# Kernel tuning notes

Hardware: AMD Instinct MI355X
Metric: run time of the kernel (lower is better)

The kernel has to match this reference:

```python
import jax, jax.numpy as jnp
import numpy as np

N, C, H, W = 4, 256, 64, 64  # in_channels == out_channels == C


def conv1x1(x, w, b):
    # x: [N, Cin, H, W], w: [Cout, Cin], b: [Cout]
    return jnp.einsum('nchw,oc->nohw', x, w) + b[None, :, None, None]


def setup_inputs() -> dict:
    key = jax.random.key(0)
    ks = jax.random.split(key, 4)
    scale = 1.0 / np.sqrt(C)
    return {
        'x': jax.random.normal(ks[0], (N, C, H, W), dtype=jnp.float32),
        'theta_w': jax.random.normal(ks[1], (C, C), dtype=jnp.float32) * scale,
        'theta_b': jnp.zeros((C,), dtype=jnp.float32),
        'phi_w': jax.random.normal(ks[2], (C, C), dtype=jnp.float32) * scale,
        'phi_b': jnp.zeros((C,), dtype=jnp.float32),
        'conv1_w': jax.random.normal(ks[3], (C, C), dtype=jnp.float32) * scale,
        'conv1_b': jnp.zeros((C,), dtype=jnp.float32),
    }


def reference(x, theta_w, theta_b, phi_w, phi_b, conv1_w, conv1_b):
    n, c, h, w = x.shape
    hw = h * w
    theta = conv1x1(x, theta_w, theta_b).reshape(n, c, hw)   # queries [N,C,HW]
    phi = conv1x1(x, phi_w, phi_b).reshape(n, c, hw)         # keys    [N,C,HW]
    g = x.reshape(n, c, hw)                                   # values  [N,C,HW]
    # f = einsum('niab,nicd->nabcd') flattened: [N, HW_q, HW_k]
    scores = jnp.einsum('ncp,ncq->npq', theta, phi) / jnp.sqrt(jnp.asarray(c, x.dtype))
    attn = jax.nn.softmax(scores, axis=-1)                    # softmax over keys
    # f = einsum('nabcd,nicd->niab'): weighted sum of values
    f = jnp.einsum('npq,ncq->ncp', attn, g).reshape(n, c, h, w)
    result = conv1x1(f, conv1_w, conv1_b)
    return x + result
```

## Files before the change

### kernel.cpp

```cpp
#include <hip/hip_runtime.h>
#include <hip/hip_bf16.h>

typedef __attribute__((ext_vector_type(8))) short short8;
typedef __attribute__((ext_vector_type(4))) short short4_t;
typedef __attribute__((ext_vector_type(4))) float float4_t;
typedef unsigned short ushort;

#define HW 4096
#define CC 256
#define NBATCH 4
#define SEQ ((size_t)NBATCH * HW)

static __device__ __forceinline__ unsigned short f2b(float f) {
    union { float f; unsigned u; } v; v.f = f;
    unsigned r = v.u + 0x7FFF + ((v.u >> 16) & 1);
    return (unsigned short)(r >> 16);
}
static __device__ __forceinline__ float b2f(unsigned short u) {
    union { unsigned u; float f; } v; v.u = ((unsigned)u) << 16;
    return v.f;
}
static __device__ __forceinline__ unsigned pk2(float a, float b) {
    __hip_bfloat162 h = __float22bfloat162_rn(make_float2(a, b));
    union { __hip_bfloat162 h; unsigned u; } v; v.h = h; return v.u;
}

static __device__ __forceinline__ void barrier_lds() {
    asm volatile("s_waitcnt lgkmcnt(0)" ::: "memory");
    __builtin_amdgcn_s_barrier();
    __builtin_amdgcn_sched_barrier(0);
}

__global__ __launch_bounds__(256) void k_prep(const float* __restrict__ x,
                                              const float* __restrict__ tw,
                                              const float* __restrict__ pw,
                                              const float* __restrict__ cw,
                                              unsigned short* __restrict__ XT,
                                              unsigned short* __restrict__ gb,
                                              unsigned short* __restrict__ Wbt,
                                              unsigned short* __restrict__ Wbp,
                                              unsigned short* __restrict__ Wbc) {
    __shared__ float T[64][65];
    int fb = blockIdx.x + 64 * (blockIdx.y + 4 * blockIdx.z);
    if (fb < 768) {
        int i = fb * 256 + threadIdx.x;
        int sel = i >> 16, off = i & 65535;
        const float* s = sel == 0 ? tw : (sel == 1 ? pw : cw);
        unsigned short* d = sel == 0 ? Wbt : (sel == 1 ? Wbp : Wbc);
        d[off] = f2b(s[off]);
    }
    int n = blockIdx.z, c0 = blockIdx.y * 64, p0 = blockIdx.x * 64;
    int t = threadIdx.x;
    int pl = t & 63, rg = t >> 6;
    const float* xp = x + ((size_t)n * CC + c0) * HW + p0;
    #pragma unroll
    for (int i = 0; i < 16; i++) {
        int cl = rg * 16 + i;
        float v = xp[(size_t)cl * HW + pl];
        T[cl][pl] = v;
        gb[((size_t)n * CC + c0 + cl) * HW + p0 + pl] = f2b(v);
    }
    __syncthreads();
    int cl = t & 63, pg = t >> 6;
    unsigned short* xt = XT + ((size_t)n * HW + p0) * CC + c0;
    #pragma unroll
    for (int i = 0; i < 16; i++) {
        int plw = pg * 16 + i;
        xt[(size_t)plw * CC + cl] = f2b(T[cl][plw]);
    }
}

__global__ __launch_bounds__(256) void k_proj(const unsigned short* __restrict__ XT,
                                              const unsigned short* __restrict__ Wt,
                                              const unsigned short* __restrict__ Wp,
                                              const float* __restrict__ bt,
                                              const float* __restrict__ bp,
                                              unsigned short* __restrict__ outT_t,
                                              unsigned short* __restrict__ outT_p) {
    const unsigned short* W; const float* b; unsigned short* outT;
    if (blockIdx.y == 0) { W = Wt; b = bt; outT = outT_t; }
    else                 { W = Wp; b = bp; outT = outT_p; }
    int w = threadIdx.x >> 6, lane = threadIdx.x & 63;
    int nidx = lane & 15, quad = lane >> 4;
    size_t row0 = (size_t)blockIdx.x * 64 + w * 16;
    float4_t acc[16];
    #pragma unroll
    for (int i = 0; i < 16; i++) acc[i] = (float4_t)(0.f);
    const unsigned short* arow = XT + (row0 + nidx) * CC + quad * 8;
    for (int ks = 0; ks < 8; ks++) {
        short8 a = *(const short8*)(arow + ks * 32);
        #pragma unroll
        for (int cb = 0; cb < 16; cb++) {
            short8 bb = *(const short8*)(W + (size_t)(cb * 16 + nidx) * CC + ks * 32 + quad * 8);
            acc[cb] = __builtin_amdgcn_mfma_f32_16x16x32_bf16(a, bb, acc[cb], 0, 0, 0);
        }
    }
    #pragma unroll
    for (int cb = 0; cb < 16; cb++) {
        int co = cb * 16 + nidx;
        float bias = b[co];
        #pragma unroll
        for (int r = 0; r < 4; r++) {
            size_t prow = row0 + quad * 4 + r;
            outT[prow * CC + co] = f2b(acc[cb][r] + bias);
        }
    }
}

__global__ __launch_bounds__(512)
void k_attn(const unsigned short* __restrict__ thetaT,
            const unsigned short* __restrict__ phiT,
            const unsigned short* __restrict__ gb,
            ushort* __restrict__ Ow, float* __restrict__ lw) {
    __shared__ __align__(16) ushort Kl[2][16384];
    __shared__ __align__(16) ushort Pbuf[2][16][64][8];
    __shared__ float Lbuf[2][128];

    const int tid = threadIdx.x;
    const int w = tid >> 6, lane = tid & 63;
    const int nidx = lane & 15, quad = lane >> 4;
    const int qg = w & 3;
    const int kh = w >> 2;
    const int nb = (blockIdx.x & 7) >> 1;
    const int h  = blockIdx.x & 1;
    const int qtile = blockIdx.x >> 3;
    const int p0 = qtile * 128;
    const size_t seq0 = (size_t)nb * HW;
    const ushort* Kg = phiT + seq0 * CC;
    const ushort* Vg = gb + (size_t)nb * CC * HW;
    const int k00 = h * 2048;

    short8 th[2][8];
    #pragma unroll
    for (int qs = 0; qs < 2; qs++) {
        const ushort* qrow = thetaT + (seq0 + p0 + qg * 32 + qs * 16 + nidx) * CC + quad * 8;
        #pragma unroll
        for (int kb = 0; kb < 8; kb++) th[qs][kb] = *(const short8*)(qrow + kb * 32);
    }

    float4_t o[2][8];
    #pragma unroll
    for (int i = 0; i < 2; i++)
        #pragma unroll
        for (int j = 0; j < 8; j++) o[i][j] = (float4_t)(0.f);
    float lrow[2] = {0.f, 0.f};

    const int c_s = tid >> 4, n_s = tid & 15;
    const int kfbase = (c_s >> 2) * 512 + ((c_s & 3) * 16 + n_s) * 8;
    auto loadKregs = [&](short8 (&kr)[4], int tt) {
        #pragma unroll
        for (int rr = 0; rr < 4; rr++)
            kr[rr] = *(const short8*)(Kg + (size_t)(k00 + tt * 64 + rr * 16 + n_s) * CC + c_s * 8);
    };
    auto stageK = [&](int buf, const short8 (&kr)[4]) {
        #pragma unroll
        for (int rr = 0; rr < 4; rr++) *(short8*)(&Kl[buf][rr * 4096 + kfbase]) = kr[rr];
    };
    auto loadVregs = [&](short8 (&vr)[4], int tt) {
        #pragma unroll
        for (int mg = 0; mg < 2; mg++)
            #pragma unroll
            for (int kst = 0; kst < 2; kst++)
                vr[mg * 2 + kst] = *(const short8*)(Vg + (size_t)(w * 32 + mg * 16 + nidx) * HW
                                                    + k00 + tt * 64 + kst * 32 + quad * 8);
    };

    const float SC = 0.0625f * 1.44269504088896f;
    const int Gp = quad >> 1;
    const int pcell_lo = (nidx ^ (Gp * 4));
    const int pj0 = (quad & 1) * 4;
    const int prcell = ((lane >> 4) << 4) | ((lane & 15) ^ (((lane >> 4) & 1) * 4));

    float4_t s00, s01, s10, s11;
    auto expPhase = [&](int buf) {
        {
            float e0 = exp2f(s00[0] * SC), e1 = exp2f(s00[1] * SC);
            float e2 = exp2f(s00[2] * SC), e3 = exp2f(s00[3] * SC);
            lrow[0] += (e0 + e1) + (e2 + e3);
            uint2 pk; pk.x = pk2(e0, e1); pk.y = pk2(e2, e3);
            *(uint2*)(&Pbuf[buf][(qg * 2 + 0) * 2 + kh][(0 * 2 + Gp) * 16 + pcell_lo][pj0]) = pk;
        }
        {
            float e0 = exp2f(s01[0] * SC), e1 = exp2f(s01[1] * SC);
            float e2 = exp2f(s01[2] * SC), e3 = exp2f(s01[3] * SC);
            lrow[1] += (e0 + e1) + (e2 + e3);
            uint2 pk; pk.x = pk2(e0, e1); pk.y = pk2(e2, e3);
            *(uint2*)(&Pbuf[buf][(qg * 2 + 1) * 2 + kh][(0 * 2 + Gp) * 16 + pcell_lo][pj0]) = pk;
        }
        {
            float e0 = exp2f(s10[0] * SC), e1 = exp2f(s10[1] * SC);
            float e2 = exp2f(s10[2] * SC), e3 = exp2f(s10[3] * SC);
            lrow[0] += (e0 + e1) + (e2 + e3);
            uint2 pk; pk.x = pk2(e0, e1); pk.y = pk2(e2, e3);
            *(uint2*)(&Pbuf[buf][(qg * 2 + 0) * 2 + kh][(1 * 2 + Gp) * 16 + pcell_lo][pj0]) = pk;
        }
        {
            float e0 = exp2f(s11[0] * SC), e1 = exp2f(s11[1] * SC);
            float e2 = exp2f(s11[2] * SC), e3 = exp2f(s11[3] * SC);
            lrow[1] += (e0 + e1) + (e2 + e3);
            uint2 pk; pk.x = pk2(e0, e1); pk.y = pk2(e2, e3);
            *(uint2*)(&Pbuf[buf][(qg * 2 + 1) * 2 + kh][(1 * 2 + Gp) * 16 + pcell_lo][pj0]) = pk;
        }
    };

    short8 kregs[4], vA[4], vB[4];

    auto ITER = [&](int t, const short8 (&vCur)[4], short8 (&vNext)[4]) {
        const int pb = t & 1;
        const int kbuf = (t + 1) & 1;
        s00 = (float4_t)(0.f); s01 = (float4_t)(0.f);
        s10 = (float4_t)(0.f); s11 = (float4_t)(0.f);
        __builtin_amdgcn_s_setprio(1);
        #pragma unroll
        for (int i = 0; i < 8; i++) {
            short8 k0 = *(const short8*)(&Kl[kbuf][((kh * 2 + 0) * 8 + i) * 512 + lane * 8]);
            short8 k1 = *(const short8*)(&Kl[kbuf][((kh * 2 + 1) * 8 + i) * 512 + lane * 8]);
            s00 = __builtin_amdgcn_mfma_f32_16x16x32_bf16(k0, th[0][i], s00, 0, 0, 0);
            s01 = __builtin_amdgcn_mfma_f32_16x16x32_bf16(k0, th[1][i], s01, 0, 0, 0);
            s10 = __builtin_amdgcn_mfma_f32_16x16x32_bf16(k1, th[0][i], s10, 0, 0, 0);
            s11 = __builtin_amdgcn_mfma_f32_16x16x32_bf16(k1, th[1][i], s11, 0, 0, 0);
            short8 pf0 = *(const short8*)(&Pbuf[pb][i * 2 + 0][prcell][0]);
            short8 pf1 = *(const short8*)(&Pbuf[pb][i * 2 + 1][prcell][0]);
            o[0][i] = __builtin_amdgcn_mfma_f32_16x16x32_bf16(vCur[0], pf0, o[0][i], 0, 0, 0);
            o[0][i] = __builtin_amdgcn_mfma_f32_16x16x32_bf16(vCur[1], pf1, o[0][i], 0, 0, 0);
            o[1][i] = __builtin_amdgcn_mfma_f32_16x16x32_bf16(vCur[2], pf0, o[1][i], 0, 0, 0);
            o[1][i] = __builtin_amdgcn_mfma_f32_16x16x32_bf16(vCur[3], pf1, o[1][i], 0, 0, 0);
        }
        __builtin_amdgcn_s_setprio(0);
        loadVregs(vNext, t + 1);
        expPhase((t + 1) & 1);
        if (t < 30) {
            stageK((t + 2) & 1, kregs);
            loadKregs(kregs, (t + 3 < 32) ? t + 3 : 31);
        }
        barrier_lds();
    };

    loadKregs(kregs, 0); loadVregs(vA, 0);
    stageK(0, kregs);
    loadKregs(kregs, 1);
    barrier_lds();
    s00 = (float4_t)(0.f); s01 = (float4_t)(0.f); s10 = (float4_t)(0.f); s11 = (float4_t)(0.f);
    __builtin_amdgcn_s_setprio(1);
    #pragma unroll
    for (int kb = 0; kb < 8; kb++) {
        short8 k0 = *(const short8*)(&Kl[0][((kh * 2 + 0) * 8 + kb) * 512 + lane * 8]);
        short8 k1 = *(const short8*)(&Kl[0][((kh * 2 + 1) * 8 + kb) * 512 + lane * 8]);
        s00 = __builtin_amdgcn_mfma_f32_16x16x32_bf16(k0, th[0][kb], s00, 0, 0, 0);
        s01 = __builtin_amdgcn_mfma_f32_16x16x32_bf16(k0, th[1][kb], s01, 0, 0, 0);
        s10 = __builtin_amdgcn_mfma_f32_16x16x32_bf16(k1, th[0][kb], s10, 0, 0, 0);
        s11 = __builtin_amdgcn_mfma_f32_16x16x32_bf16(k1, th[1][kb], s11, 0, 0, 0);
    }
    __builtin_amdgcn_s_setprio(0);
    expPhase(0);
    stageK(1, kregs);
    loadKregs(kregs, 2);
    barrier_lds();

    #pragma unroll 1
    for (int tt = 0; tt < 15; tt++) {
        ITER(tt * 2, vA, vB);
        ITER(tt * 2 + 1, vB, vA);
    }
    ITER(30, vA, vB);
    #pragma unroll
    for (int i = 0; i < 8; i++) {
        short8 pf0 = *(const short8*)(&Pbuf[1][i * 2 + 0][prcell][0]);
        short8 pf1 = *(const short8*)(&Pbuf[1][i * 2 + 1][prcell][0]);
        o[0][i] = __builtin_amdgcn_mfma_f32_16x16x32_bf16(vB[0], pf0, o[0][i], 0, 0, 0);
        o[0][i] = __builtin_amdgcn_mfma_f32_16x16x32_bf16(vB[1], pf1, o[0][i], 0, 0, 0);
        o[1][i] = __builtin_amdgcn_mfma_f32_16x16x32_bf16(vB[2], pf0, o[1][i], 0, 0, 0);
        o[1][i] = __builtin_amdgcn_mfma_f32_16x16x32_bf16(vB[3], pf1, o[1][i], 0, 0, 0);
    }

    #pragma unroll
    for (int qs = 0; qs < 2; qs++) {
        float v = lrow[qs];
        v += __shfl_xor(v, 16);
        v += __shfl_xor(v, 32);
        if (quad == 0) Lbuf[kh][qg * 32 + qs * 16 + nidx] = v;
    }
    __syncthreads();
    if (tid < 128)
        lw[(size_t)h * SEQ + seq0 + p0 + tid] = Lbuf[0][tid] + Lbuf[1][tid];
    ushort* Op = Ow + ((size_t)h * SEQ + seq0 + p0) * CC;
    #pragma unroll
    for (int mg = 0; mg < 2; mg++)
        #pragma unroll
        for (int qq = 0; qq < 8; qq++) {
            uint2 pk;
            pk.x = pk2(o[mg][qq][0], o[mg][qq][1]);
            pk.y = pk2(o[mg][qq][2], o[mg][qq][3]);
            *(uint2*)(Op + (size_t)(qq * 16 + nidx) * CC + w * 32 + mg * 16 + quad * 4) = pk;
        }
}

__global__ __launch_bounds__(512)
void k_final(const unsigned short* __restrict__ Wc,
             const float* __restrict__ bc,
             const ushort* __restrict__ Ow,
             const float* __restrict__ lw,
             const float* __restrict__ x,
             float* __restrict__ out) {
    __shared__ __align__(16) ushort F[64][256];
    const int n = blockIdx.z;
    const int p0 = blockIdx.x * 64;
    const int tid = threadIdx.x;

    {
        const int r = tid >> 3;
        const int c0 = tid & 7;
        const size_t grow = (size_t)n * HW + p0 + r;
        const float li = 1.0f / (lw[grow] + lw[SEQ + grow]);
        const short8* O0 = (const short8*)(Ow + grow * CC);
        const short8* O1 = (const short8*)(Ow + SEQ * CC + grow * CC);
        #pragma unroll
        for (int i = 0; i < 4; i++) {
            int ch = c0 + 8 * i;
            short8 a = O0[ch];
            short8 b = O1[ch];
            union { short8 s; unsigned u[4]; } pk;
            float f[8];
            #pragma unroll
            for (int j = 0; j < 8; j++)
                f[j] = (b2f((ushort)a[j]) + b2f((ushort)b[j])) * li;
            pk.u[0] = pk2(f[0], f[1]); pk.u[1] = pk2(f[2], f[3]);
            pk.u[2] = pk2(f[4], f[5]); pk.u[3] = pk2(f[6], f[7]);
            int swz = ch ^ (r & 7);
            *(short8*)(&F[r][swz * 8]) = pk.s;
        }
    }
    __syncthreads();

    const int w = tid >> 6, lane = tid & 63;
    const int nidx = lane & 15, quad = lane >> 4;
    const int co_base = w * 32;
    float4_t acc[2][4];
    #pragma unroll
    for (int i = 0; i < 2; i++)
        #pragma unroll
        for (int j = 0; j < 4; j++) acc[i][j] = (float4_t)(0.f);

    const unsigned short* a0row = Wc + (size_t)(co_base + nidx) * CC + quad * 8;
    const unsigned short* a1row = Wc + (size_t)(co_base + 16 + nidx) * CC + quad * 8;
    for (int ks = 0; ks < 8; ks++) {
        short8 a0 = *(const short8*)(a0row + ks * 32);
        short8 a1 = *(const short8*)(a1row + ks * 32);
        #pragma unroll
        for (int pb = 0; pb < 4; pb++) {
            int row = pb * 16 + nidx;
            int chunk = (ks * 4 + quad) ^ (row & 7);
            short8 bb = *(const short8*)(&F[row][chunk * 8]);
            acc[0][pb] = __builtin_amdgcn_mfma_f32_16x16x32_bf16(a0, bb, acc[0][pb], 0, 0, 0);
            acc[1][pb] = __builtin_amdgcn_mfma_f32_16x16x32_bf16(a1, bb, acc[1][pb], 0, 0, 0);
        }
    }

    #pragma unroll
    for (int cb = 0; cb < 2; cb++) {
        #pragma unroll
        for (int pb = 0; pb < 4; pb++) {
            #pragma unroll
            for (int r2 = 0; r2 < 4; r2++) {
                int co = co_base + cb * 16 + quad * 4 + r2;
                size_t idx = ((size_t)n * CC + co) * HW + p0 + pb * 16 + nidx;
                out[idx] = x[idx] + bc[co] + acc[cb][pb][r2];
            }
        }
    }
}

extern "C" void kernel_launch(void* const* d_in, const int* in_sizes, int n_in,
                              void* d_out, int out_size, void* d_ws, size_t ws_size,
                              hipStream_t stream) {
    const float* x       = (const float*)d_in[0];
    const float* theta_w = (const float*)d_in[1];
    const float* theta_b = (const float*)d_in[2];
    const float* phi_w   = (const float*)d_in[3];
    const float* phi_b   = (const float*)d_in[4];
    const float* conv1_w = (const float*)d_in[5];
    const float* conv1_b = (const float*)d_in[6];
    float* out = (float*)d_out;

    unsigned short* XT  = (unsigned short*)d_ws;
    unsigned short* gb  = XT  + SEQ * CC;
    unsigned short* thT = gb  + SEQ * CC;
    unsigned short* phT = thT + SEQ * CC;
    unsigned short* fT  = phT + SEQ * CC;
    unsigned short* Wbt = fT  + SEQ * CC;
    unsigned short* Wbp = Wbt + 65536;
    unsigned short* Wbc = Wbp + 65536;
    unsigned short* Ow  = Wbc + 65536;
    float* lw = (float*)(Ow + 2 * SEQ * CC);

    k_prep<<<dim3(64, 4, 4), 256, 0, stream>>>(x, theta_w, phi_w, conv1_w, XT, gb, Wbt, Wbp, Wbc);
    k_proj<<<dim3(256, 2), 256, 0, stream>>>(XT, Wbt, Wbp, theta_b, phi_b, thT, phT);
    k_attn<<<dim3(256), 512, 0, stream>>>(thT, phT, gb, Ow, lw);
    k_final<<<dim3(64, 1, 4), 512, 0, stream>>>(Wbc, conv1_b, Ow, lw, x, out);
}
```

Measured before the change: 203.4 us.

## Fuse x transpose/cast with theta/phi projections and convert weights inline

Merges the prep and projection kernels into one. Each block stages a 64-pixel tile of x, transposed and swizzled, in LDS and runs both the theta and phi 1x1 convolutions on it, so the XT intermediate never goes through global memory. Weights are now read as fp32 and packed to bf16 inside the projection and final kernels, which removes the separate weight-conversion pass. The attention kernel also drops its s_setprio hints and swaps its custom LDS barrier for __syncthreads. The fused kernel launches only 256 blocks, fewer than the old projection launch, and repeats the weight reads and conversion in every block.

```diff
diff --git a/kernel.cpp b/kernel.cpp
--- a/kernel.cpp
+++ b/kernel.cpp
@@ -25,85 +25,90 @@
     union { __hip_bfloat162 h; unsigned u; } v; v.h = h; return v.u;
 }
 
-static __device__ __forceinline__ void barrier_lds() {
-    asm volatile("s_waitcnt lgkmcnt(0)" ::: "memory");
-    __builtin_amdgcn_s_barrier();
-    __builtin_amdgcn_sched_barrier(0);
-}
-
-__global__ __launch_bounds__(256) void k_prep(const float* __restrict__ x,
-                                              const float* __restrict__ tw,
-                                              const float* __restrict__ pw,
-                                              const float* __restrict__ cw,
-                                              unsigned short* __restrict__ XT,
-                                              unsigned short* __restrict__ gb,
-                                              unsigned short* __restrict__ Wbt,
-                                              unsigned short* __restrict__ Wbp,
-                                              unsigned short* __restrict__ Wbc) {
+__global__ __launch_bounds__(512)
+void k_pp(const float* __restrict__ x,
+          const float* __restrict__ tw, const float* __restrict__ pw,
+          const float* __restrict__ thb, const float* __restrict__ phb,
+          unsigned short* __restrict__ gb,
+          unsigned short* __restrict__ thT, unsigned short* __restrict__ phT) {
     __shared__ float T[64][65];
-    int fb = blockIdx.x + 64 * (blockIdx.y + 4 * blockIdx.z);
-    if (fb < 768) {
-        int i = fb * 256 + threadIdx.x;
-        int sel = i >> 16, off = i & 65535;
-        const float* s = sel == 0 ? tw : (sel == 1 ? pw : cw);
-        unsigned short* d = sel == 0 ? Wbt : (sel == 1 ? Wbp : Wbc);
-        d[off] = f2b(s[off]);
-    }
-    int n = blockIdx.z, c0 = blockIdx.y * 64, p0 = blockIdx.x * 64;
-    int t = threadIdx.x;
-    int pl = t & 63, rg = t >> 6;
-    const float* xp = x + ((size_t)n * CC + c0) * HW + p0;
-    #pragma unroll
-    for (int i = 0; i < 16; i++) {
-        int cl = rg * 16 + i;
-        float v = xp[(size_t)cl * HW + pl];
-        T[cl][pl] = v;
-        gb[((size_t)n * CC + c0 + cl) * HW + p0 + pl] = f2b(v);
-    }
-    __syncthreads();
-    int cl = t & 63, pg = t >> 6;
-    unsigned short* xt = XT + ((size_t)n * HW + p0) * CC + c0;
-    #pragma unroll
-    for (int i = 0; i < 16; i++) {
-        int plw = pg * 16 + i;
-        xt[(size_t)plw * CC + cl] = f2b(T[cl][plw]);
-    }
-}
-
-__global__ __launch_bounds__(256) void k_proj(const unsigned short* __restrict__ XT,
-                                              const unsigned short* __restrict__ Wt,
-                                              const unsigned short* __restrict__ Wp,
-                                              const float* __restrict__ bt,
-                                              const float* __restrict__ bp,
-                                              unsigned short* __restrict__ outT_t,
-                                              unsigned short* __restrict__ outT_p) {
-    const unsigned short* W; const float* b; unsigned short* outT;
-    if (blockIdx.y == 0) { W = Wt; b = bt; outT = outT_t; }
-    else                 { W = Wp; b = bp; outT = outT_p; }
-    int w = threadIdx.x >> 6, lane = threadIdx.x & 63;
-    int nidx = lane & 15, quad = lane >> 4;
-    size_t row0 = (size_t)blockIdx.x * 64 + w * 16;
-    float4_t acc[16];
-    #pragma unroll
-    for (int i = 0; i < 16; i++) acc[i] = (float4_t)(0.f);
-    const unsigned short* arow = XT + (row0 + nidx) * CC + quad * 8;
+    __shared__ __align__(16) ushort F[64][256];
+    const int n = blockIdx.z;
+    const int p0 = blockIdx.x * 64;
+    const int tid = threadIdx.x;
+
+    {
+        const int pl = tid & 63, rg = tid >> 6;
+        for (int cc = 0; cc < 4; cc++) {
+            const int c0 = cc * 64;
+            const float* xp = x + ((size_t)n * CC + c0) * HW + p0;
+            #pragma unroll
+            for (int i = 0; i < 8; i++) {
+                int cl = rg * 8 + i;
+                float v = xp[(size_t)cl * HW + pl];
+                T[cl][pl] = v;
+                gb[((size_t)n * CC + c0 + cl) * HW + p0 + pl] = f2b(v);
+            }
+            __syncthreads();
+            const int cl2 = tid & 63, pg = tid >> 6;
+            #pragma unroll
+            for (int i = 0; i < 8; i++) {
+                int plw = pg * 8 + i;
+                int c = c0 + cl2;
+                int swz = (c >> 3) ^ (plw & 7);
+                F[plw][swz * 8 + (c & 7)] = f2b(T[cl2][plw]);
+            }
+            __syncthreads();
+        }
+    }
+
+    const int w = tid >> 6, lane = tid & 63;
+    const int nidx = lane & 15, quad = lane >> 4;
+    const float* Wsel = (w < 4) ? tw : pw;
+    const float* bsel = (w < 4) ? thb : phb;
+    unsigned short* osel = (w < 4) ? thT : phT;
+    const int cq = w & 3;
+
+    float4_t acc[4][4];
+    #pragma unroll
+    for (int i = 0; i < 4; i++)
+        #pragma unroll
+        for (int j = 0; j < 4; j++) acc[i][j] = (float4_t)(0.f);
+
     for (int ks = 0; ks < 8; ks++) {
-        short8 a = *(const short8*)(arow + ks * 32);
-        #pragma unroll
-        for (int cb = 0; cb < 16; cb++) {
-            short8 bb = *(const short8*)(W + (size_t)(cb * 16 + nidx) * CC + ks * 32 + quad * 8);
-            acc[cb] = __builtin_amdgcn_mfma_f32_16x16x32_bf16(a, bb, acc[cb], 0, 0, 0);
-        }
-    }
-    #pragma unroll
-    for (int cb = 0; cb < 16; cb++) {
-        int co = cb * 16 + nidx;
-        float bias = b[co];
-        #pragma unroll
-        for (int r = 0; r < 4; r++) {
-            size_t prow = row0 + quad * 4 + r;
-            outT[prow * CC + co] = f2b(acc[cb][r] + bias);
-        }
+        short8 af[4];
+        #pragma unroll
+        for (int mt = 0; mt < 4; mt++) {
+            int row = mt * 16 + nidx;
+            int chn = (ks * 4 + quad) ^ (row & 7);
+            af[mt] = *(const short8*)(&F[row][chn * 8]);
+        }
+        #pragma unroll
+        for (int cb = 0; cb < 4; cb++) {
+            int co = cq * 64 + cb * 16 + nidx;
+            const float* wp = Wsel + (size_t)co * CC + ks * 32 + quad * 8;
+            float4_t w0 = *(const float4_t*)(wp);
+            float4_t w1 = *(const float4_t*)(wp + 4);
+            union { short8 s; unsigned u[4]; } bfr;
+            bfr.u[0] = pk2(w0[0], w0[1]); bfr.u[1] = pk2(w0[2], w0[3]);
+            bfr.u[2] = pk2(w1[0], w1[1]); bfr.u[3] = pk2(w1[2], w1[3]);
+            #pragma unroll
+            for (int mt = 0; mt < 4; mt++)
+                acc[mt][cb] = __builtin_amdgcn_mfma_f32_16x16x32_bf16(af[mt], bfr.s, acc[mt][cb], 0, 0, 0);
+        }
+    }
+
+    #pragma unroll
+    for (int cb = 0; cb < 4; cb++) {
+        int co = cq * 64 + cb * 16 + nidx;
+        float bias = bsel[co];
+        #pragma unroll
+        for (int mt = 0; mt < 4; mt++)
+            #pragma unroll
+            for (int r = 0; r < 4; r++) {
+                size_t prow = (size_t)n * HW + p0 + mt * 16 + quad * 4 + r;
+                osel[prow * CC + co] = f2b(acc[mt][cb][r] + bias);
+            }
     }
 }
 
@@ -210,7 +215,6 @@
         const int kbuf = (t + 1) & 1;
         s00 = (float4_t)(0.f); s01 = (float4_t)(0.f);
         s10 = (float4_t)(0.f); s11 = (float4_t)(0.f);
-        __builtin_amdgcn_s_setprio(1);
         #pragma unroll
         for (int i = 0; i < 8; i++) {
             short8 k0 = *(const short8*)(&Kl[kbuf][((kh * 2 + 0) * 8 + i) * 512 + lane * 8]);
@@ -226,22 +230,20 @@
             o[1][i] = __builtin_amdgcn_mfma_f32_16x16x32_bf16(vCur[2], pf0, o[1][i], 0, 0, 0);
             o[1][i] = __builtin_amdgcn_mfma_f32_16x16x32_bf16(vCur[3], pf1, o[1][i], 0, 0, 0);
         }
-        __builtin_amdgcn_s_setprio(0);
         loadVregs(vNext, t + 1);
         expPhase((t + 1) & 1);
         if (t < 30) {
             stageK((t + 2) & 1, kregs);
             loadKregs(kregs, (t + 3 < 32) ? t + 3 : 31);
         }
-        barrier_lds();
+        __syncthreads();
     };
 
     loadKregs(kregs, 0); loadVregs(vA, 0);
     stageK(0, kregs);
     loadKregs(kregs, 1);
-    barrier_lds();
+    __syncthreads();
     s00 = (float4_t)(0.f); s01 = (float4_t)(0.f); s10 = (float4_t)(0.f); s11 = (float4_t)(0.f);
-    __builtin_amdgcn_s_setprio(1);
     #pragma unroll
     for (int kb = 0; kb < 8; kb++) {
         short8 k0 = *(const short8*)(&Kl[0][((kh * 2 + 0) * 8 + kb) * 512 + lane * 8]);
@@ -251,11 +253,10 @@
         s10 = __builtin_amdgcn_mfma_f32_16x16x32_bf16(k1, th[0][kb], s10, 0, 0, 0);
         s11 = __builtin_amdgcn_mfma_f32_16x16x32_bf16(k1, th[1][kb], s11, 0, 0, 0);
     }
-    __builtin_amdgcn_s_setprio(0);
     expPhase(0);
     stageK(1, kregs);
     loadKregs(kregs, 2);
-    barrier_lds();
+    __syncthreads();
 
     #pragma unroll 1
     for (int tt = 0; tt < 15; tt++) {
@@ -296,7 +297,7 @@
 }
 
 __global__ __launch_bounds__(512)
-void k_final(const unsigned short* __restrict__ Wc,
+void k_final(const float* __restrict__ cw,
              const float* __restrict__ bc,
              const ushort* __restrict__ Ow,
              const float* __restrict__ lw,
@@ -341,18 +342,25 @@
         #pragma unroll
         for (int j = 0; j < 4; j++) acc[i][j] = (float4_t)(0.f);
 
-    const unsigned short* a0row = Wc + (size_t)(co_base + nidx) * CC + quad * 8;
-    const unsigned short* a1row = Wc + (size_t)(co_base + 16 + nidx) * CC + quad * 8;
+    const float* a0row = cw + (size_t)(co_base + nidx) * CC + quad * 8;
+    const float* a1row = cw + (size_t)(co_base + 16 + nidx) * CC + quad * 8;
     for (int ks = 0; ks < 8; ks++) {
-        short8 a0 = *(const short8*)(a0row + ks * 32);
-        short8 a1 = *(const short8*)(a1row + ks * 32);
+        float4_t w00 = *(const float4_t*)(a0row + ks * 32);
+        float4_t w01 = *(const float4_t*)(a0row + ks * 32 + 4);
+        float4_t w10 = *(const float4_t*)(a1row + ks * 32);
+        float4_t w11 = *(const float4_t*)(a1row + ks * 32 + 4);
+        union { short8 s; unsigned u[4]; } a0, a1;
+        a0.u[0] = pk2(w00[0], w00[1]); a0.u[1] = pk2(w00[2], w00[3]);
+        a0.u[2] = pk2(w01[0], w01[1]); a0.u[3] = pk2(w01[2], w01[3]);
+        a1.u[0] = pk2(w10[0], w10[1]); a1.u[1] = pk2(w10[2], w10[3]);
+        a1.u[2] = pk2(w11[0], w11[1]); a1.u[3] = pk2(w11[2], w11[3]);
         #pragma unroll
         for (int pb = 0; pb < 4; pb++) {
             int row = pb * 16 + nidx;
             int chunk = (ks * 4 + quad) ^ (row & 7);
             short8 bb = *(const short8*)(&F[row][chunk * 8]);
-            acc[0][pb] = __builtin_amdgcn_mfma_f32_16x16x32_bf16(a0, bb, acc[0][pb], 0, 0, 0);
-            acc[1][pb] = __builtin_amdgcn_mfma_f32_16x16x32_bf16(a1, bb, acc[1][pb], 0, 0, 0);
+            acc[0][pb] = __builtin_amdgcn_mfma_f32_16x16x32_bf16(a0.s, bb, acc[0][pb], 0, 0, 0);
+            acc[1][pb] = __builtin_amdgcn_mfma_f32_16x16x32_bf16(a1.s, bb, acc[1][pb], 0, 0, 0);
         }
     }
 
@@ -382,19 +390,13 @@
     const float* conv1_b = (const float*)d_in[6];
     float* out = (float*)d_out;
 
-    unsigned short* XT  = (unsigned short*)d_ws;
-    unsigned short* gb  = XT  + SEQ * CC;
+    unsigned short* gb  = (unsigned short*)d_ws;
     unsigned short* thT = gb  + SEQ * CC;
     unsigned short* phT = thT + SEQ * CC;
-    unsigned short* fT  = phT + SEQ * CC;
-    unsigned short* Wbt = fT  + SEQ * CC;
-    unsigned short* Wbp = Wbt + 65536;
-    unsigned short* Wbc = Wbp + 65536;
-    unsigned short* Ow  = Wbc + 65536;
+    unsigned short* Ow  = phT + SEQ * CC;
     float* lw = (float*)(Ow + 2 * SEQ * CC);
 
-    k_prep<<<dim3(64, 4, 4), 256, 0, stream>>>(x, theta_w, phi_w, conv1_w, XT, gb, Wbt, Wbp, Wbc);
-    k_proj<<<dim3(256, 2), 256, 0, stream>>>(XT, Wbt, Wbp, theta_b, phi_b, thT, phT);
+    k_pp<<<dim3(64, 1, 4), 512, 0, stream>>>(x, theta_w, phi_w, theta_b, phi_b, gb, thT, phT);
     k_attn<<<dim3(256), 512, 0, stream>>>(thT, phT, gb, Ow, lw);
-    k_final<<<dim3(64, 1, 4), 512, 0, stream>>>(Wbc, conv1_b, Ow, lw, x, out);
-}
+    k_final<<<dim3(64, 1, 4), 512, 0, stream>>>(conv1_w, conv1_b, Ow, lw, x, out);
+}
```

New measurement: 185.1 us (median of 3 runs). 9.0% less time.
